# Kernel tuning notes

Hardware: AMD Instinct MI355X
Metric: run time of the kernel (lower is better)

## Reference

```python
import jax, jax.numpy as jnp
import numpy as np

N_NODES = 50000
N_EDGES = 800000
LATDIM = 128
HEAD = 4


def setup_inputs() -> dict:
    key = jax.random.key(0)
    k1, k2, k3, k4, k5, k6 = jax.random.split(key, 6)
    scale = 1.0 / np.sqrt(LATDIM)  # xavier-ish scale for the square projections
    return {
        "embeds": jax.random.normal(k1, (N_NODES, LATDIM), dtype=jnp.float32),
        "qW": jax.random.normal(k2, (LATDIM, LATDIM), dtype=jnp.float32) * scale,
        "kW": jax.random.normal(k3, (LATDIM, LATDIM), dtype=jnp.float32) * scale,
        "vW": jax.random.normal(k4, (LATDIM, LATDIM), dtype=jnp.float32) * scale,
        "rows": jax.random.randint(k5, (N_EDGES,), 0, N_NODES, dtype=jnp.int32),
        "cols": jax.random.randint(k6, (N_EDGES,), 0, N_NODES, dtype=jnp.int32),
    }


def reference(embeds, qW, kW, vW, rows, cols):
    n_nodes, latdim = embeds.shape
    head_dim = latdim // HEAD
    rowEmb = embeds[rows]                         # [E, D] gather by dst
    colEmb = embeds[cols]                         # [E, D] gather by src
    q = (rowEmb @ qW).reshape(-1, HEAD, head_dim)  # [E, H, Dh]
    k = (colEmb @ kW).reshape(-1, HEAD, head_dim)
    v = (colEmb @ vW).reshape(-1, HEAD, head_dim)
    att = jnp.einsum('ehd,ehd->eh', q, k)
    att = jnp.clip(att, -10.0, 10.0)
    expAtt = jnp.exp(att)                          # [E, H]
    # segment softmax denominator via scatter-add over destination nodes
    attNorm = jax.ops.segment_sum(expAtt, rows, num_segments=n_nodes)[rows]
    att = expAtt / (attNorm + 1e-8)
    res = (att[:, :, None] * v).reshape(-1, latdim)  # [E, D]
    out = jax.ops.segment_sum(res, rows, num_segments=n_nodes)  # [N, D]
    return out
```

## Files before the change

### kernel.cpp

```cpp
#include <hip/hip_runtime.h>
#include <hip/hip_bf16.h>

#define N_NODES 50000
#define N_EDGES 800000
#define LATDIM 128
#define HEAD 4
#define SLOT_CAP 96

typedef __attribute__((ext_vector_type(8))) short short8;
typedef __attribute__((ext_vector_type(4))) float floatx4;

__device__ __forceinline__ unsigned bf16_rne_bits(float x) {
    unsigned u = __builtin_bit_cast(unsigned, x);
    return (u + 0x7fffu + ((u >> 16) & 1u)) & 0xffff0000u;
}
__device__ __forceinline__ void split_bf16(float x, short& hi, short& lo) {
    unsigned hb = bf16_rne_bits(x);
    hi = (short)(hb >> 16);
    float hf = __builtin_bit_cast(float, hb);
    unsigned lb = bf16_rne_bits(x - hf);
    lo = (short)(lb >> 16);
}

#define SCAT_BLOCKS ((N_EDGES / 4 + 255) / 256)

__global__ __launch_bounds__(256) void prep_kernel(
    const float* __restrict__ qW, const float* __restrict__ kW,
    const float* __restrict__ vW,
    short* __restrict__ Whi, short* __restrict__ Wlo,
    const int* __restrict__ rows, const int* __restrict__ cols,
    int* __restrict__ cnt, int* __restrict__ slots)
{
    const int b = blockIdx.x;
    if (b < 192) {
        const int which = b >> 6;
        const float* W = (which == 0) ? qW : (which == 1) ? kW : vW;
        const int t = (b & 63) * 256 + threadIdx.x;
        const int k = t >> 7, n = t & 127;
        const int c = k >> 5, q = (k >> 3) & 3, j = k & 7;
        short hi, lo;
        split_bf16(W[k * 128 + n], hi, lo);
        const int dst = which * 16384 + ((c * 128 + n) * 4 + q) * 8 + j;
        Whi[dst] = hi;
        Wlo[dst] = lo;
    } else {
        const int t = (b - 192) * 256 + threadIdx.x;
        if (t < N_EDGES / 4) {
            int4 r = ((const int4*)rows)[t];
            int4 c = ((const int4*)cols)[t];
            int p;
            p = atomicAdd(&cnt[r.x], 1);
            if (p < SLOT_CAP) slots[(size_t)r.x * SLOT_CAP + p] = c.x;
            p = atomicAdd(&cnt[r.y], 1);
            if (p < SLOT_CAP) slots[(size_t)r.y * SLOT_CAP + p] = c.y;
            p = atomicAdd(&cnt[r.z], 1);
            if (p < SLOT_CAP) slots[(size_t)r.z * SLOT_CAP + p] = c.z;
            p = atomicAdd(&cnt[r.w], 1);
            if (p < SLOT_CAP) slots[(size_t)r.w * SLOT_CAP + p] = c.w;
        }
    }
}

#define GEMM_BLOCKS ((N_NODES + 63) / 64)
#define LDSP 136

__global__ __launch_bounds__(768) void gemm_kernel(
    const float* __restrict__ E,
    const short* __restrict__ Whi, const short* __restrict__ Wlo,
    float* __restrict__ Q, unsigned short* __restrict__ KV2)
{
    __shared__ short AhL[64 * LDSP];
    __shared__ short AlL[64 * LDSP];

    const int r_base = blockIdx.x * 64;

    for (int chnk = threadIdx.x; chnk < 2048; chnk += 768) {
        const int row = chnk >> 5, c4 = chnk & 31;
        int grow = r_base + row;
        if (grow > N_NODES - 1) grow = N_NODES - 1;
        float4 x = ((const float4*)E)[(size_t)grow * 32 + c4];
        short h0, l0, h1, l1, h2, l2, h3, l3;
        split_bf16(x.x, h0, l0);
        split_bf16(x.y, h1, l1);
        split_bf16(x.z, h2, l2);
        split_bf16(x.w, h3, l3);
        *(short4*)(AhL + row * LDSP + c4 * 4) = make_short4(h0, h1, h2, h3);
        *(short4*)(AlL + row * LDSP + c4 * 4) = make_short4(l0, l1, l2, l3);
    }
    __syncthreads();

    const int wave = threadIdx.x >> 6;
    const int lane = threadIdx.x & 63;
    const int which = wave >> 2;
    const int n_base = (wave & 3) * 32;
    const int ln = lane & 15;
    const int q  = lane >> 4;

    short8 Bh[2][4], Bl[2][4];
#pragma unroll
    for (int tIdx = 0; tIdx < 2; ++tIdx)
#pragma unroll
        for (int c = 0; c < 4; ++c) {
            const int off = which * 16384 +
                            ((c * 128 + n_base + tIdx * 16 + ln) * 4 + q) * 8;
            Bh[tIdx][c] = *(const short8*)(Whi + off);
            Bl[tIdx][c] = *(const short8*)(Wlo + off);
        }

    const int vs = (which == 2) ? 32 : 0;
    const int c0 = n_base + ln;
    const int c1 = n_base + 16 + ln;

    for (int rt = 0; rt < 4; ++rt) {
        const short* ah = AhL + (rt * 16 + ln) * LDSP + q * 8;
        const short* al = AlL + (rt * 16 + ln) * LDSP + q * 8;

        floatx4 acc0 = {0.f, 0.f, 0.f, 0.f};
        floatx4 acc1 = {0.f, 0.f, 0.f, 0.f};
#pragma unroll
        for (int c = 0; c < 4; ++c) {
            short8 Ah = *(const short8*)(ah + c * 32);
            short8 Al = *(const short8*)(al + c * 32);
            acc0 = __builtin_amdgcn_mfma_f32_16x16x32_bf16(Ah, Bh[0][c], acc0, 0, 0, 0);
            acc0 = __builtin_amdgcn_mfma_f32_16x16x32_bf16(Ah, Bl[0][c], acc0, 0, 0, 0);
            acc0 = __builtin_amdgcn_mfma_f32_16x16x32_bf16(Al, Bh[0][c], acc0, 0, 0, 0);
            acc1 = __builtin_amdgcn_mfma_f32_16x16x32_bf16(Ah, Bh[1][c], acc1, 0, 0, 0);
            acc1 = __builtin_amdgcn_mfma_f32_16x16x32_bf16(Ah, Bl[1][c], acc1, 0, 0, 0);
            acc1 = __builtin_amdgcn_mfma_f32_16x16x32_bf16(Al, Bh[1][c], acc1, 0, 0, 0);
        }

        const int r0 = r_base + rt * 16;
#pragma unroll
        for (int r = 0; r < 4; ++r) {
            const int row = r0 + q * 4 + r;
            if (row >= N_NODES) continue;
            if (which == 0) {
                Q[(size_t)row * 128 + c0] = acc0[r];
                Q[(size_t)row * 128 + c1] = acc1[r];
            } else {
                KV2[(size_t)row * 256 + (c0 >> 5) * 64 + (c0 & 31) + vs] =
                    (unsigned short)(bf16_rne_bits(acc0[r]) >> 16);
                KV2[(size_t)row * 256 + (c1 >> 5) * 64 + (c1 & 31) + vs] =
                    (unsigned short)(bf16_rne_bits(acc1[r]) >> 16);
            }
        }
    }
}

__global__ __launch_bounds__(256) void fused_kernel(
    const float* __restrict__ Q,
    const unsigned short* __restrict__ KV2,
    const int* __restrict__ cnt,
    const int* __restrict__ slots,
    float* __restrict__ out)
{
    const int n = blockIdx.x * 4 + (threadIdx.x >> 6);
    if (n >= N_NODES) return;
    const int lane = threadIdx.x & 63;
    const int s  = lane & 1;
    const int h  = (lane >> 1) & 3;
    const int el = lane >> 3;

    int deg = cnt[n];
    if (deg > SLOT_CAP) deg = SLOT_CAP;

    float qv[16];
    {
        const float4* qp = (const float4*)(Q + (size_t)n * 128 + h * 32 + s * 16);
#pragma unroll
        for (int j = 0; j < 4; ++j) {
            float4 t = qp[j];
            qv[4 * j + 0] = t.x; qv[4 * j + 1] = t.y;
            qv[4 * j + 2] = t.z; qv[4 * j + 3] = t.w;
        }
    }

    float acc[16];
#pragma unroll
    for (int j = 0; j < 16; ++j) acc[j] = 0.f;
    float norm = 0.f;

    const int* srow = slots + (size_t)n * SLOT_CAP;

    for (int i = 0; i < deg; i += 8) {
        const int e = i + el;
        if (e < deg) {
            const int col = srow[e];
            const unsigned short* kp = KV2 + (size_t)col * 256 + h * 64 + s * 16;
            uint4 k0 = *(const uint4*)(kp);
            uint4 k1 = *(const uint4*)(kp + 8);
            uint4 v0 = *(const uint4*)(kp + 32);
            uint4 v1 = *(const uint4*)(kp + 40);

            unsigned kw[8] = {k0.x, k0.y, k0.z, k0.w, k1.x, k1.y, k1.z, k1.w};
            float p = 0.f;
#pragma unroll
            for (int d = 0; d < 8; ++d) {
                float flo = __builtin_bit_cast(float, kw[d] << 16);
                float fhi = __builtin_bit_cast(float, kw[d] & 0xffff0000u);
                p += qv[2 * d] * flo + qv[2 * d + 1] * fhi;
            }
            p += __shfl_xor(p, 1);

            float a = expf(fminf(fmaxf(p, -10.0f), 10.0f));
            norm += a;

            unsigned vw[8] = {v0.x, v0.y, v0.z, v0.w, v1.x, v1.y, v1.z, v1.w};
#pragma unroll
            for (int d = 0; d < 8; ++d) {
                float flo = __builtin_bit_cast(float, vw[d] << 16);
                float fhi = __builtin_bit_cast(float, vw[d] & 0xffff0000u);
                acc[2 * d]     += a * flo;
                acc[2 * d + 1] += a * fhi;
            }
        }
    }

#pragma unroll
    for (int m = 8; m <= 32; m <<= 1) {
        norm += __shfl_xor(norm, m, 64);
#pragma unroll
        for (int j = 0; j < 16; ++j) acc[j] += __shfl_xor(acc[j], m, 64);
    }

    if (el == 0) {
        const float inv = 1.0f / (norm + 1e-8f);
        float4* op = (float4*)(out + (size_t)n * 128 + h * 32 + s * 16);
#pragma unroll
        for (int j = 0; j < 4; ++j)
            op[j] = make_float4(acc[4 * j] * inv, acc[4 * j + 1] * inv,
                                acc[4 * j + 2] * inv, acc[4 * j + 3] * inv);
    }
}

extern "C" void kernel_launch(void* const* d_in, const int* in_sizes, int n_in,
                              void* d_out, int out_size, void* d_ws, size_t ws_size,
                              hipStream_t stream) {
    const float* embeds = (const float*)d_in[0];
    const float* qW     = (const float*)d_in[1];
    const float* kW     = (const float*)d_in[2];
    const float* vW     = (const float*)d_in[3];
    const int*   rows   = (const int*)d_in[4];
    const int*   cols   = (const int*)d_in[5];
    float* out = (float*)d_out;

    float* Q = (float*)d_ws;
    unsigned short* KV2 = (unsigned short*)(Q + (size_t)N_NODES * LATDIM);
    int* cnt   = (int*)(KV2 + (size_t)N_NODES * 256);
    int* slots = cnt + N_NODES;
    short* Whi = (short*)(slots + (size_t)N_NODES * SLOT_CAP);
    short* Wlo = Whi + 3 * 16384;

    hipMemsetAsync(cnt, 0, sizeof(int) * N_NODES, stream);

    prep_kernel<<<192 + SCAT_BLOCKS, 256, 0, stream>>>(
        qW, kW, vW, Whi, Wlo, rows, cols, cnt, slots);

    gemm_kernel<<<GEMM_BLOCKS, 768, 0, stream>>>(embeds, Whi, Wlo, Q, KV2);

    fused_kernel<<<(N_NODES + 3) / 4, 256, 0, stream>>>(
        Q, KV2, cnt, slots, out);
}
```

Baseline: 220.7 us.

## Merge weight prep and edge scatter into GEMM kernel, split weights per block

The separate prep kernel is removed. Edge bucketing now runs in extra leading blocks of the GEMM launch, and each GEMM wave loads and splits its fp32 weight fragment into bf16 hi/lo directly in registers. This saves one kernel launch and the workspace round-trip for the pre-split weights, and lets the scatter atomics overlap with GEMM work. In exchange, every GEMM block repeats the weight conversion with strided scalar fp32 loads instead of vector loads of pre-packed data.

Measured after the change: 211.9 us. 4.0% less time.

```diff
diff --git a/kernel.cpp b/kernel.cpp
--- a/kernel.cpp
+++ b/kernel.cpp
@@ -22,29 +22,23 @@
     lo = (short)(lb >> 16);
 }
 
-#define SCAT_BLOCKS ((N_EDGES / 4 + 255) / 256)
-
-__global__ __launch_bounds__(256) void prep_kernel(
+#define SCAT_T ((N_EDGES / 4 + 767) / 768)
+#define GEMM_BLOCKS ((N_NODES + 63) / 64)
+#define LDSP 136
+
+__global__ __launch_bounds__(768) void gemm_scatter_kernel(
+    const float* __restrict__ E,
     const float* __restrict__ qW, const float* __restrict__ kW,
     const float* __restrict__ vW,
-    short* __restrict__ Whi, short* __restrict__ Wlo,
     const int* __restrict__ rows, const int* __restrict__ cols,
-    int* __restrict__ cnt, int* __restrict__ slots)
+    int* __restrict__ cnt, int* __restrict__ slots,
+    float* __restrict__ Q, unsigned short* __restrict__ KV2)
 {
-    const int b = blockIdx.x;
-    if (b < 192) {
-        const int which = b >> 6;
-        const float* W = (which == 0) ? qW : (which == 1) ? kW : vW;
-        const int t = (b & 63) * 256 + threadIdx.x;
-        const int k = t >> 7, n = t & 127;
-        const int c = k >> 5, q = (k >> 3) & 3, j = k & 7;
-        short hi, lo;
-        split_bf16(W[k * 128 + n], hi, lo);
-        const int dst = which * 16384 + ((c * 128 + n) * 4 + q) * 8 + j;
-        Whi[dst] = hi;
-        Wlo[dst] = lo;
-    } else {
-        const int t = (b - 192) * 256 + threadIdx.x;
+    __shared__ short AhL[64 * LDSP];
+    __shared__ short AlL[64 * LDSP];
+
+    if (blockIdx.x < SCAT_T) {
+        const int t = blockIdx.x * 768 + threadIdx.x;
         if (t < N_EDGES / 4) {
             int4 r = ((const int4*)rows)[t];
             int4 c = ((const int4*)cols)[t];
@@ -58,21 +52,10 @@
             p = atomicAdd(&cnt[r.w], 1);
             if (p < SLOT_CAP) slots[(size_t)r.w * SLOT_CAP + p] = c.w;
         }
-    }
-}
-
-#define GEMM_BLOCKS ((N_NODES + 63) / 64)
-#define LDSP 136
-
-__global__ __launch_bounds__(768) void gemm_kernel(
-    const float* __restrict__ E,
-    const short* __restrict__ Whi, const short* __restrict__ Wlo,
-    float* __restrict__ Q, unsigned short* __restrict__ KV2)
-{
-    __shared__ short AhL[64 * LDSP];
-    __shared__ short AlL[64 * LDSP];
-
-    const int r_base = blockIdx.x * 64;
+        return;
+    }
+
+    const int r_base = (blockIdx.x - SCAT_T) * 64;
 
     for (int chnk = threadIdx.x; chnk < 2048; chnk += 768) {
         const int row = chnk >> 5, c4 = chnk & 31;
@@ -87,7 +70,6 @@
         *(short4*)(AhL + row * LDSP + c4 * 4) = make_short4(h0, h1, h2, h3);
         *(short4*)(AlL + row * LDSP + c4 * 4) = make_short4(l0, l1, l2, l3);
     }
-    __syncthreads();
 
     const int wave = threadIdx.x >> 6;
     const int lane = threadIdx.x & 63;
@@ -96,16 +78,22 @@
     const int ln = lane & 15;
     const int q  = lane >> 4;
 
+    const float* W = (which == 0) ? qW : (which == 1) ? kW : vW;
     short8 Bh[2][4], Bl[2][4];
 #pragma unroll
     for (int tIdx = 0; tIdx < 2; ++tIdx)
 #pragma unroll
-        for (int c = 0; c < 4; ++c) {
-            const int off = which * 16384 +
-                            ((c * 128 + n_base + tIdx * 16 + ln) * 4 + q) * 8;
-            Bh[tIdx][c] = *(const short8*)(Whi + off);
-            Bl[tIdx][c] = *(const short8*)(Wlo + off);
-        }
+        for (int c = 0; c < 4; ++c)
+#pragma unroll
+            for (int j = 0; j < 8; ++j) {
+                float w = W[(c * 32 + q * 8 + j) * 128 + n_base + tIdx * 16 + ln];
+                short hi, lo;
+                split_bf16(w, hi, lo);
+                Bh[tIdx][c][j] = hi;
+                Bl[tIdx][c][j] = lo;
+            }
+
+    __syncthreads();
 
     const int vs = (which == 2) ? 32 : 0;
     const int c0 = n_base + ln;
@@ -248,15 +236,11 @@
     unsigned short* KV2 = (unsigned short*)(Q + (size_t)N_NODES * LATDIM);
     int* cnt   = (int*)(KV2 + (size_t)N_NODES * 256);
     int* slots = cnt + N_NODES;
-    short* Whi = (short*)(slots + (size_t)N_NODES * SLOT_CAP);
-    short* Wlo = Whi + 3 * 16384;
 
     hipMemsetAsync(cnt, 0, sizeof(int) * N_NODES, stream);
 
-    prep_kernel<<<192 + SCAT_BLOCKS, 256, 0, stream>>>(
-        qW, kW, vW, Whi, Wlo, rows, cols, cnt, slots);
-
-    gemm_kernel<<<GEMM_BLOCKS, 768, 0, stream>>>(embeds, Whi, Wlo, Q, KV2);
+    gemm_scatter_kernel<<<SCAT_T + GEMM_BLOCKS, 768, 0, stream>>>(
+        embeds, qW, kW, vW, rows, cols, cnt, slots, Q, KV2);
 
     fused_kernel<<<(N_NODES + 3) / 4, 256, 0, stream>>>(
         Q, KV2, cnt, slots, out);
```
